# Performance work log

Hardware: AMD Instinct MI355X
Metric: run time of the kernel (lower is better)

## Reference

```python
import jax, jax.numpy as jnp
import numpy as np
import math

B, T, D, K, V = 8, 2048, 512, 512, 512


def setup_inputs() -> dict:
    key = jax.random.key(0)
    ks = jax.random.split(key, 4)
    minibatch = jax.random.normal(ks[0], (B, T, D), dtype=jnp.float32)
    # nn.Linear weights are [out, in]; biases [out]
    Wk = jax.random.normal(ks[1], (K, D), dtype=jnp.float32) * 0.02
    bk = jnp.zeros((K,), dtype=jnp.float32)
    Wq = jax.random.normal(ks[2], (K, D), dtype=jnp.float32) * 0.02
    bq = jnp.zeros((K,), dtype=jnp.float32)
    Wv = jax.random.normal(ks[3], (V, D), dtype=jnp.float32) * 0.02
    bv = jnp.zeros((V,), dtype=jnp.float32)
    return {"minibatch": minibatch, "Wk": Wk, "bk": bk, "Wq": Wq, "bq": bq, "Wv": Wv, "bv": bv}


def reference(minibatch, Wk, bk, Wq, bq, Wv, bv):
    k_size = Wk.shape[0]
    sqrt_k = math.sqrt(k_size)
    keys = jnp.einsum('btd,kd->btk', minibatch, Wk) + bk
    queries = jnp.einsum('btd,kd->btk', minibatch, Wq) + bq
    values = jnp.einsum('btd,vd->btv', minibatch, Wv) + bv
    # logits[b, t, s] = q_t . k_s
    logits = jnp.einsum('btk,bsk->bts', queries, keys)
    seq = minibatch.shape[1]
    # upper triangle (s > t) masked to -inf, matching np.triu(..., k=1)
    mask = jnp.triu(jnp.ones((seq, seq), dtype=bool), k=1)
    logits = jnp.where(mask[None, :, :], -jnp.inf, logits)
    # NOTE: original softmaxes over dim=1 (the query axis), then divides by sqrt(k)
    probs = jax.nn.softmax(logits, axis=1) / sqrt_k
    read = jnp.einsum('bts,bsv->btv', probs, values)
    return minibatch + read
```

## Files before the change

### kernel.cpp

```cpp
#include <hip/hip_runtime.h>


typedef __attribute__((ext_vector_type(4))) float f32x4;
typedef __attribute__((ext_vector_type(8))) short s16x8;
typedef __attribute__((ext_vector_type(4))) short s16x4;

#define SQRTK  22.627416997969522f

__device__ __forceinline__ short f2bf(float f) {
    union { float f; unsigned int i; } c; c.f = f;
    unsigned int x = c.i;
    return (short)((x + 0x7fffu + ((x >> 16) & 1u)) >> 16);
}
__device__ __forceinline__ void gll16(const void* g, void* l) {
    __builtin_amdgcn_global_load_lds(
        (const __attribute__((address_space(1))) void*)g,
        (__attribute__((address_space(3))) void*)l, 16, 0, 0);
}

__global__ __launch_bounds__(256) void k_cast(
    const float* __restrict__ in, unsigned short* __restrict__ out, int n4)
{
    int i = blockIdx.x * 256 + threadIdx.x;
    if (i >= n4) return;
    f32x4 v = *(const f32x4*)(in + (size_t)i * 4);
    s16x4 o;
#pragma unroll
    for (int j = 0; j < 4; ++j) o[j] = f2bf(v[j]);
    *(s16x4*)(out + (size_t)i * 4) = o;
}

__global__ __launch_bounds__(256) void k_castw(
    const float* __restrict__ q, const float* __restrict__ k, const float* __restrict__ v,
    unsigned short* __restrict__ oqk, unsigned short* __restrict__ ov)
{
    int i = blockIdx.x * 256 + threadIdx.x;
    const float* src; unsigned short* dst; int j;
    if (i < 65536)       { src = q; dst = oqk; j = i; }
    else if (i < 131072) { src = k; dst = oqk + 262144; j = i - 65536; }
    else                 { src = v; dst = ov; j = i - 131072; }
    f32x4 w = *(const f32x4*)(src + (size_t)j * 4);
    s16x4 o;
#pragma unroll
    for (int jj = 0; jj < 4; ++jj) o[jj] = f2bf(w[jj]);
    *(s16x4*)(dst + (size_t)j * 4) = o;
}

__global__ __launch_bounds__(256) void k_projqk(
    const unsigned short* __restrict__ Xb,
    const unsigned short* __restrict__ Wqk,
    const float* __restrict__ bq, const float* __restrict__ bk,
    unsigned short* __restrict__ C)
{
    __shared__ short la[2][128][32];
    __shared__ short lb[2][128][32];
    const int tid  = threadIdx.x;
    const int wave = tid >> 6, lane = tid & 63;
    const int wr = (wave >> 1) * 64, wc = (wave & 1) * 64;
    const int m0 = blockIdx.x * 128, n0 = blockIdx.y * 128;
    const int r0 = tid >> 2, c0 = (tid & 3) * 8;
    const int wvb = wave * 1024;
    const int frl = lane & 15, kb = (lane >> 4) * 8, rg4 = (lane >> 4) * 4;
    f32x4 acc[4][4] = {};

#define QK_STAGE(BUF, K0) { \
    char* pa_ = (char*)(&la[BUF][0][0]) + wvb; \
    char* pb_ = (char*)(&lb[BUF][0][0]) + wvb; \
    gll16(Xb  + (size_t)(m0 + r0) * 512 + (K0) + c0, pa_); \
    gll16(Xb  + (size_t)(m0 + r0 + 64) * 512 + (K0) + c0, pa_ + 4096); \
    gll16(Wqk + (size_t)(n0 + r0) * 512 + (K0) + c0, pb_); \
    gll16(Wqk + (size_t)(n0 + r0 + 64) * 512 + (K0) + c0, pb_ + 4096); }

    QK_STAGE(0, 0);
    __syncthreads();
    for (int ks = 0; ks < 16; ++ks) {
        const int cur = ks & 1;
        if (ks < 15) QK_STAGE(cur ^ 1, (ks + 1) * 32);
        s16x8 af[4], bfr[4];
#pragma unroll
        for (int i = 0; i < 4; ++i) af[i]  = *(const s16x8*)(&la[cur][wr + i * 16 + frl][kb]);
#pragma unroll
        for (int i = 0; i < 4; ++i) bfr[i] = *(const s16x8*)(&lb[cur][wc + i * 16 + frl][kb]);
#pragma unroll
        for (int mi = 0; mi < 4; ++mi)
#pragma unroll
            for (int ni = 0; ni < 4; ++ni)
                acc[mi][ni] = __builtin_amdgcn_mfma_f32_16x16x32_bf16(af[mi], bfr[ni], acc[mi][ni], 0, 0, 0);
        __syncthreads();
    }
#undef QK_STAGE
#pragma unroll
    for (int mi = 0; mi < 4; ++mi)
#pragma unroll
        for (int ni = 0; ni < 4; ++ni) {
            int col = n0 + wc + ni * 16 + frl;
            float bv = (col < 512) ? bq[col] : bk[col - 512];
#pragma unroll
            for (int r = 0; r < 4; ++r) {
                int row = m0 + wr + mi * 16 + rg4 + r;
                C[(size_t)row * 1024 + col] = f2bf(acc[mi][ni][r] + bv);
            }
        }
}

__global__ __launch_bounds__(256) void k_projv(
    const unsigned short* __restrict__ Wv,
    const unsigned short* __restrict__ Xb,
    const float* __restrict__ bv,
    const float* __restrict__ ft,
    unsigned short* __restrict__ C)
{
    __shared__ short la[2][128][32];
    __shared__ short lb[2][128][32];
    const int tid  = threadIdx.x;
    const int wave = tid >> 6, lane = tid & 63;
    const int wr = (wave >> 1) * 64, wc = (wave & 1) * 64;
    const int m0 = blockIdx.x * 128, n0 = blockIdx.y * 128;
    const int r0 = tid >> 2, c0 = (tid & 3) * 8;
    const int wvb = wave * 1024;
    const int frl = lane & 15, kb = (lane >> 4) * 8, rg4 = (lane >> 4) * 4;
    f32x4 acc[4][4] = {};

#define PV_STAGE(BUF, K0) { \
    char* pa_ = (char*)(&la[BUF][0][0]) + wvb; \
    char* pb_ = (char*)(&lb[BUF][0][0]) + wvb; \
    gll16(Wv + (size_t)(m0 + r0) * 512 + (K0) + c0, pa_); \
    gll16(Wv + (size_t)(m0 + r0 + 64) * 512 + (K0) + c0, pa_ + 4096); \
    gll16(Xb + (size_t)(n0 + r0) * 512 + (K0) + c0, pb_); \
    gll16(Xb + (size_t)(n0 + r0 + 64) * 512 + (K0) + c0, pb_ + 4096); }

    PV_STAGE(0, 0);
    __syncthreads();
    for (int ks = 0; ks < 16; ++ks) {
        const int cur = ks & 1;
        if (ks < 15) PV_STAGE(cur ^ 1, (ks + 1) * 32);
        s16x8 af[4], bfr[4];
#pragma unroll
        for (int i = 0; i < 4; ++i) af[i]  = *(const s16x8*)(&la[cur][wr + i * 16 + frl][kb]);
#pragma unroll
        for (int i = 0; i < 4; ++i) bfr[i] = *(const s16x8*)(&lb[cur][wc + i * 16 + frl][kb]);
#pragma unroll
        for (int mi = 0; mi < 4; ++mi)
#pragma unroll
            for (int ni = 0; ni < 4; ++ni)
                acc[mi][ni] = __builtin_amdgcn_mfma_f32_16x16x32_bf16(af[mi], bfr[ni], acc[mi][ni], 0, 0, 0);
        __syncthreads();
    }
#undef PV_STAGE
#pragma unroll
    for (int mi = 0; mi < 4; ++mi)
#pragma unroll
        for (int ni = 0; ni < 4; ++ni) {
            int col = n0 + wc + ni * 16 + frl;
            float fs = ft[col];
#pragma unroll
            for (int r = 0; r < 4; ++r) {
                int row = m0 + wr + mi * 16 + rg4 + r;
                C[(size_t)row * 16384 + col] = f2bf((acc[mi][ni][r] + bv[row]) * fs);
            }
        }
}

__global__ __launch_bounds__(256) void k_logits(
    const unsigned short* __restrict__ QK,
    unsigned short* __restrict__ Pc,
    float* __restrict__ pz)
{
    const int n = blockIdx.x;
    const int b = n & 7;
    const int p = n >> 3;
    int tt = (int)((sqrtf(8.f * p + 1.f) - 1.f) * 0.5f);
    while ((tt + 1) * (tt + 2) / 2 <= p) ++tt;
    while (tt * (tt + 1) / 2 > p) --tt;
    const int st = p - tt * (tt + 1) / 2;
    const int t0 = tt * 128, s0 = st * 128;

    const unsigned short* A  = QK + (size_t)b * 2048 * 1024;
    const unsigned short* Bt = QK + (size_t)b * 2048 * 1024 + 512;
    unsigned short* Pb = Pc + (size_t)b * 2048 * 2048;

    __shared__ short la[2][128][32];
    __shared__ short lb[2][128][32];
    __shared__ float sz[2][128];
    const int tid  = threadIdx.x;
    const int wave = tid >> 6, lane = tid & 63;
    const int wr = (wave >> 1) * 64, wc = (wave & 1) * 64;
    const int r0 = tid >> 2, c0 = (tid & 3) * 8;
    const int wvb = wave * 1024;
    const int frl = lane & 15, kb = (lane >> 4) * 8, rg4 = (lane >> 4) * 4;
    f32x4 acc[4][4] = {};

#define LG_STAGE(BUF, K0) { \
    char* pa_ = (char*)(&la[BUF][0][0]) + wvb; \
    char* pb_ = (char*)(&lb[BUF][0][0]) + wvb; \
    gll16(A  + (size_t)(t0 + r0) * 1024 + (K0) + c0, pa_); \
    gll16(A  + (size_t)(t0 + r0 + 64) * 1024 + (K0) + c0, pa_ + 4096); \
    gll16(Bt + (size_t)(s0 + r0) * 1024 + (K0) + c0, pb_); \
    gll16(Bt + (size_t)(s0 + r0 + 64) * 1024 + (K0) + c0, pb_ + 4096); }

    LG_STAGE(0, 0);
    __syncthreads();
    for (int ks = 0; ks < 16; ++ks) {
        const int cur = ks & 1;
        if (ks < 15) LG_STAGE(cur ^ 1, (ks + 1) * 32);
        s16x8 af[4], bfr[4];
#pragma unroll
        for (int i = 0; i < 4; ++i) af[i]  = *(const s16x8*)(&la[cur][wr + i * 16 + frl][kb]);
#pragma unroll
        for (int i = 0; i < 4; ++i) bfr[i] = *(const s16x8*)(&lb[cur][wc + i * 16 + frl][kb]);
#pragma unroll
        for (int mi = 0; mi < 4; ++mi)
#pragma unroll
            for (int ni = 0; ni < 4; ++ni)
                acc[mi][ni] = __builtin_amdgcn_mfma_f32_16x16x32_bf16(af[mi], bfr[ni], acc[mi][ni], 0, 0, 0);
        __syncthreads();
    }
#undef LG_STAGE

    float cz[4];
#pragma unroll
    for (int ni = 0; ni < 4; ++ni) {
        const int colg = s0 + wc + ni * 16 + frl;
        float zl = 0.f;
#pragma unroll
        for (int mi = 0; mi < 4; ++mi)
#pragma unroll
            for (int r = 0; r < 4; ++r) {
                int row = t0 + wr + mi * 16 + rg4 + r;
                float e = (colg <= row) ? __expf(acc[mi][ni][r]) : 0.f;
                acc[mi][ni][r] = e;
                zl += e;
            }
        zl += __shfl_xor(zl, 16);
        zl += __shfl_xor(zl, 32);
        cz[ni] = zl;
    }
    if (lane < 16) {
#pragma unroll
        for (int ni = 0; ni < 4; ++ni)
            sz[wr >> 6][wc + ni * 16 + lane] = cz[ni];
    }
    __syncthreads();
    if (tid < 128)
        pz[(b * 16 + tt) * 2048 + s0 + tid] = sz[0][tid] + sz[1][tid];
#pragma unroll
    for (int ni = 0; ni < 4; ++ni) {
        const int colg = s0 + wc + ni * 16 + frl;
#pragma unroll
        for (int mi = 0; mi < 4; ++mi)
#pragma unroll
            for (int r = 0; r < 4; ++r) {
                int row = t0 + wr + mi * 16 + rg4 + r;
                Pb[(size_t)row * 2048 + colg] = f2bf(acc[mi][ni][r]);
            }
    }
}

__global__ __launch_bounds__(256) void k_stats2(
    const float* __restrict__ pz, float* __restrict__ ft)
{
    const int i = blockIdx.x * 256 + threadIdx.x;
    const int b = i >> 11, s = i & 2047;
    float Z = 0.f;
    for (int tc = s >> 7; tc < 16; ++tc) Z += pz[(b * 16 + tc) * 2048 + s];
    ft[i] = 1.0f / (Z * SQRTK);
}

__global__ __launch_bounds__(256) void k_out(
    const unsigned short* __restrict__ Pc,
    const unsigned short* __restrict__ Vs,
    const float* __restrict__ X,
    float* __restrict__ Y)
{
    __shared__ short la[2][2][128][32];
    __shared__ short lb[2][2][128][32];
    const int n  = blockIdx.x;
    const int tt = 15 - (n >> 5);
    const int bv = n & 31;
    const int b = bv >> 2, v = bv & 3;
    const int t0 = tt * 128, v0 = v * 128;
    const unsigned short* Pb = Pc + (size_t)b * 2048 * 2048;
    const int tid  = threadIdx.x;
    const int wave = tid >> 6, lane = tid & 63;
    const int wr = (wave >> 1) * 64, wc = (wave & 1) * 64;
    const int frl = lane & 15, kb = (lane >> 4) * 8, rg4 = (lane >> 4) * 4;
    const int r0 = tid >> 2, c0 = (tid & 3) * 8;
    const int wvb = wave * 1024;

    f32x4 acc[4][4] = {};
    const int nit = (tt + 1) * 2;

#define OUT_STAGE(BUF, IT) { \
    int sb = (IT) * 64; \
    _Pragma("unroll") for (int h = 0; h < 2; ++h) { \
        char* pa_ = (char*)(&la[BUF][h][0][0]) + wvb; \
        char* pb_ = (char*)(&lb[BUF][h][0][0]) + wvb; \
        gll16(Pb + (size_t)(t0 + r0) * 2048 + sb + h * 32 + c0, pa_); \
        gll16(Pb + (size_t)(t0 + r0 + 64) * 2048 + sb + h * 32 + c0, pa_ + 4096); \
        gll16(Vs + (size_t)(v0 + r0) * 16384 + b * 2048 + sb + h * 32 + c0, pb_); \
        gll16(Vs + (size_t)(v0 + r0 + 64) * 16384 + b * 2048 + sb + h * 32 + c0, pb_ + 4096); } }

    OUT_STAGE(0, 0);
    __syncthreads();
    for (int it = 0; it < nit; ++it) {
        const int cur = it & 1;
        if (it + 1 < nit) OUT_STAGE(cur ^ 1, it + 1);
#pragma unroll
        for (int h = 0; h < 2; ++h) {
            s16x8 af[4], bfr[4];
#pragma unroll
            for (int i = 0; i < 4; ++i) af[i]  = *(const s16x8*)(&la[cur][h][wr + i * 16 + frl][kb]);
#pragma unroll
            for (int i = 0; i < 4; ++i) bfr[i] = *(const s16x8*)(&lb[cur][h][wc + i * 16 + frl][kb]);
#pragma unroll
            for (int mi = 0; mi < 4; ++mi)
#pragma unroll
                for (int ni = 0; ni < 4; ++ni)
                    acc[mi][ni] = __builtin_amdgcn_mfma_f32_16x16x32_bf16(af[mi], bfr[ni], acc[mi][ni], 0, 0, 0);
        }
        __syncthreads();
    }
#undef OUT_STAGE

#pragma unroll
    for (int mi = 0; mi < 4; ++mi)
#pragma unroll
        for (int ni = 0; ni < 4; ++ni) {
            int col = v0 + wc + ni * 16 + frl;
#pragma unroll
            for (int r = 0; r < 4; ++r) {
                int row = t0 + wr + mi * 16 + rg4 + r;
                size_t o = ((size_t)b * 2048 + row) * 512 + col;
                Y[o] = acc[mi][ni][r] + X[o];
            }
        }
}

extern "C" void kernel_launch(void* const* d_in, const int* in_sizes, int n_in,
                              void* d_out, int out_size, void* d_ws, size_t ws_size,
                              hipStream_t stream) {
    const float* Xf  = (const float*)d_in[0];
    const float* Wkf = (const float*)d_in[1];
    const float* bkf = (const float*)d_in[2];
    const float* Wqf = (const float*)d_in[3];
    const float* bqf = (const float*)d_in[4];
    const float* Wvf = (const float*)d_in[5];
    const float* bvf = (const float*)d_in[6];
    float* Y = (float*)d_out;
    char* ws = (char*)d_ws;

    float*          pz   = (float*)(ws);
    float*          ftab = (float*)(ws + 2097152);
    unsigned short* Wqkb = (unsigned short*)(ws + 4194304);
    unsigned short* Wvb  = (unsigned short*)(ws + 5242880);
    unsigned short* Xb   = (unsigned short*)(ws + 6291456);
    unsigned short* QKb  = (unsigned short*)(ws + 23068672);
    unsigned short* Vs   = (unsigned short*)(ws + 56623104);
    unsigned short* Pc   = (unsigned short*)(ws + 73400320);

    dim3 blk(256);
    k_cast<<<dim3(8192), blk, 0, stream>>>(Xf, Xb, 2097152);
    k_castw<<<dim3(768), blk, 0, stream>>>(Wqf, Wkf, Wvf, Wqkb, Wvb);
    k_projqk<<<dim3(128, 8), blk, 0, stream>>>(Xb, Wqkb, bqf, bkf, QKb);
    k_logits<<<dim3(1088), blk, 0, stream>>>(QKb, Pc, pz);
    k_stats2<<<dim3(64), blk, 0, stream>>>(pz, ftab);
    k_projv<<<dim3(4, 128), blk, 0, stream>>>(Wvb, Xb, bvf, ftab, Vs);
    k_out<<<dim3(512), blk, 0, stream>>>(Pc, Vs, Xf, Y);
}
```

Measured before the change: 144.5 us.

## Triple-buffer LDS pipeline with vmcnt waits in logits and output GEMMs

Replaces the double-buffered global_load_lds loops in k_logits and k_out with a three-stage ring buffer that prefetches two K-steps ahead. Each iteration waits only on the older loads through a partial s_waitcnt vmcnt plus a single s_barrier, instead of a full __syncthreads. k_out now uses 32-wide K steps instead of 64, which roughly halves its LDS footprint but doubles the iteration count and barrier frequency. MFMA blocks are wrapped in s_setprio to favour the math waves. The goal is to hide global-to-LDS latency behind compute, at the cost of relying on hand-counted vmcnt values that must match the four loads issued per stage.

```diff
diff --git a/kernel.cpp b/kernel.cpp
--- a/kernel.cpp
+++ b/kernel.cpp
@@ -179,8 +179,8 @@
     const unsigned short* Bt = QK + (size_t)b * 2048 * 1024 + 512;
     unsigned short* Pb = Pc + (size_t)b * 2048 * 2048;
 
-    __shared__ short la[2][128][32];
-    __shared__ short lb[2][128][32];
+    __shared__ short la[3][128][32];
+    __shared__ short lb[3][128][32];
     __shared__ float sz[2][128];
     const int tid  = threadIdx.x;
     const int wave = tid >> 6, lane = tid & 63;
@@ -199,21 +199,28 @@
     gll16(Bt + (size_t)(s0 + r0 + 64) * 1024 + (K0) + c0, pb_ + 4096); }
 
     LG_STAGE(0, 0);
-    __syncthreads();
+    LG_STAGE(1, 32);
+    int cur = 0;
     for (int ks = 0; ks < 16; ++ks) {
-        const int cur = ks & 1;
-        if (ks < 15) LG_STAGE(cur ^ 1, (ks + 1) * 32);
+        if (ks < 15) { asm volatile("s_waitcnt vmcnt(4)" ::: "memory"); }
+        else         { asm volatile("s_waitcnt vmcnt(0)" ::: "memory"); }
+        __builtin_amdgcn_sched_barrier(0);
+        __builtin_amdgcn_s_barrier();
+        __builtin_amdgcn_sched_barrier(0);
+        if (ks < 14) { int nb = cur + 2; if (nb >= 3) nb -= 3; LG_STAGE(nb, (ks + 2) * 32); }
         s16x8 af[4], bfr[4];
 #pragma unroll
         for (int i = 0; i < 4; ++i) af[i]  = *(const s16x8*)(&la[cur][wr + i * 16 + frl][kb]);
 #pragma unroll
         for (int i = 0; i < 4; ++i) bfr[i] = *(const s16x8*)(&lb[cur][wc + i * 16 + frl][kb]);
+        __builtin_amdgcn_s_setprio(1);
 #pragma unroll
         for (int mi = 0; mi < 4; ++mi)
 #pragma unroll
             for (int ni = 0; ni < 4; ++ni)
                 acc[mi][ni] = __builtin_amdgcn_mfma_f32_16x16x32_bf16(af[mi], bfr[ni], acc[mi][ni], 0, 0, 0);
-        __syncthreads();
+        __builtin_amdgcn_s_setprio(0);
+        cur = (cur == 2) ? 0 : cur + 1;
     }
 #undef LG_STAGE
 
@@ -272,8 +279,8 @@
     const float* __restrict__ X,
     float* __restrict__ Y)
 {
-    __shared__ short la[2][2][128][32];
-    __shared__ short lb[2][2][128][32];
+    __shared__ short la[3][128][32];
+    __shared__ short lb[3][128][32];
     const int n  = blockIdx.x;
     const int tt = 15 - (n >> 5);
     const int bv = n & 31;
@@ -288,37 +295,40 @@
     const int wvb = wave * 1024;
 
     f32x4 acc[4][4] = {};
-    const int nit = (tt + 1) * 2;
-
-#define OUT_STAGE(BUF, IT) { \
-    int sb = (IT) * 64; \
-    _Pragma("unroll") for (int h = 0; h < 2; ++h) { \
-        char* pa_ = (char*)(&la[BUF][h][0][0]) + wvb; \
-        char* pb_ = (char*)(&lb[BUF][h][0][0]) + wvb; \
-        gll16(Pb + (size_t)(t0 + r0) * 2048 + sb + h * 32 + c0, pa_); \
-        gll16(Pb + (size_t)(t0 + r0 + 64) * 2048 + sb + h * 32 + c0, pa_ + 4096); \
-        gll16(Vs + (size_t)(v0 + r0) * 16384 + b * 2048 + sb + h * 32 + c0, pb_); \
-        gll16(Vs + (size_t)(v0 + r0 + 64) * 16384 + b * 2048 + sb + h * 32 + c0, pb_ + 4096); } }
+    const int nit = (tt + 1) * 4;
+
+#define OUT_STAGE(BUF, IS) { \
+    int sb = (IS) * 32; \
+    char* pa_ = (char*)(&la[BUF][0][0]) + wvb; \
+    char* pb_ = (char*)(&lb[BUF][0][0]) + wvb; \
+    gll16(Pb + (size_t)(t0 + r0) * 2048 + sb + c0, pa_); \
+    gll16(Pb + (size_t)(t0 + r0 + 64) * 2048 + sb + c0, pa_ + 4096); \
+    gll16(Vs + (size_t)(v0 + r0) * 16384 + b * 2048 + sb + c0, pb_); \
+    gll16(Vs + (size_t)(v0 + r0 + 64) * 16384 + b * 2048 + sb + c0, pb_ + 4096); }
 
     OUT_STAGE(0, 0);
-    __syncthreads();
+    OUT_STAGE(1, 1);
+    int cur = 0;
     for (int it = 0; it < nit; ++it) {
-        const int cur = it & 1;
-        if (it + 1 < nit) OUT_STAGE(cur ^ 1, it + 1);
-#pragma unroll
-        for (int h = 0; h < 2; ++h) {
-            s16x8 af[4], bfr[4];
-#pragma unroll
-            for (int i = 0; i < 4; ++i) af[i]  = *(const s16x8*)(&la[cur][h][wr + i * 16 + frl][kb]);
-#pragma unroll
-            for (int i = 0; i < 4; ++i) bfr[i] = *(const s16x8*)(&lb[cur][h][wc + i * 16 + frl][kb]);
-#pragma unroll
-            for (int mi = 0; mi < 4; ++mi)
-#pragma unroll
-                for (int ni = 0; ni < 4; ++ni)
-                    acc[mi][ni] = __builtin_amdgcn_mfma_f32_16x16x32_bf16(af[mi], bfr[ni], acc[mi][ni], 0, 0, 0);
-        }
-        __syncthreads();
+        if (it + 1 < nit) { asm volatile("s_waitcnt vmcnt(4)" ::: "memory"); }
+        else              { asm volatile("s_waitcnt vmcnt(0)" ::: "memory"); }
+        __builtin_amdgcn_sched_barrier(0);
+        __builtin_amdgcn_s_barrier();
+        __builtin_amdgcn_sched_barrier(0);
+        if (it + 2 < nit) { int nb = cur + 2; if (nb >= 3) nb -= 3; OUT_STAGE(nb, it + 2); }
+        s16x8 af[4], bfr[4];
+#pragma unroll
+        for (int i = 0; i < 4; ++i) af[i]  = *(const s16x8*)(&la[cur][wr + i * 16 + frl][kb]);
+#pragma unroll
+        for (int i = 0; i < 4; ++i) bfr[i] = *(const s16x8*)(&lb[cur][wc + i * 16 + frl][kb]);
+        __builtin_amdgcn_s_setprio(1);
+#pragma unroll
+        for (int mi = 0; mi < 4; ++mi)
+#pragma unroll
+            for (int ni = 0; ni < 4; ++ni)
+                acc[mi][ni] = __builtin_amdgcn_mfma_f32_16x16x32_bf16(af[mi], bfr[ni], acc[mi][ni], 0, 0, 0);
+        __builtin_amdgcn_s_setprio(0);
+        cur = (cur == 2) ? 0 : cur + 1;
     }
 #undef OUT_STAGE
 
```

After: 151.3 us. 1.05x slower.

## Overlap next-tile global loads with MFMA via partial vmcnt waits

Applied to the files above, without the earlier changes.

In the logits and output GEMM loops, the full __syncthreads after the prefetch is replaced by an explicit s_waitcnt vmcnt(N). Each iteration waits only for the current buffer's async LDS loads, so the next stage's loads stay in flight during the MFMAs. Raw s_barrier with sched_barrier fences keep the compiler from reordering around the sync points, and s_setprio raises wave priority during MFMA bursts. This relies on the hand-counted vmcnt values matching the number of issued gll16 loads, which is fragile if load counts change.

```diff
diff --git a/kernel.cpp b/kernel.cpp
--- a/kernel.cpp
+++ b/kernel.cpp
@@ -199,21 +199,32 @@
     gll16(Bt + (size_t)(s0 + r0 + 64) * 1024 + (K0) + c0, pb_ + 4096); }
 
     LG_STAGE(0, 0);
-    __syncthreads();
     for (int ks = 0; ks < 16; ++ks) {
         const int cur = ks & 1;
-        if (ks < 15) LG_STAGE(cur ^ 1, (ks + 1) * 32);
+        if (ks < 15) {
+            LG_STAGE(cur ^ 1, (ks + 1) * 32);
+            asm volatile("s_waitcnt vmcnt(4)" ::: "memory");
+        } else {
+            asm volatile("s_waitcnt vmcnt(0)" ::: "memory");
+        }
+        __builtin_amdgcn_sched_barrier(0);
+        __builtin_amdgcn_s_barrier();
+        __builtin_amdgcn_sched_barrier(0);
         s16x8 af[4], bfr[4];
 #pragma unroll
         for (int i = 0; i < 4; ++i) af[i]  = *(const s16x8*)(&la[cur][wr + i * 16 + frl][kb]);
 #pragma unroll
         for (int i = 0; i < 4; ++i) bfr[i] = *(const s16x8*)(&lb[cur][wc + i * 16 + frl][kb]);
+        __builtin_amdgcn_s_setprio(1);
 #pragma unroll
         for (int mi = 0; mi < 4; ++mi)
 #pragma unroll
             for (int ni = 0; ni < 4; ++ni)
                 acc[mi][ni] = __builtin_amdgcn_mfma_f32_16x16x32_bf16(af[mi], bfr[ni], acc[mi][ni], 0, 0, 0);
-        __syncthreads();
+        __builtin_amdgcn_s_setprio(0);
+        __builtin_amdgcn_sched_barrier(0);
+        __builtin_amdgcn_s_barrier();
+        __builtin_amdgcn_sched_barrier(0);
     }
 #undef LG_STAGE
 
@@ -301,10 +312,17 @@
         gll16(Vs + (size_t)(v0 + r0 + 64) * 16384 + b * 2048 + sb + h * 32 + c0, pb_ + 4096); } }
 
     OUT_STAGE(0, 0);
-    __syncthreads();
     for (int it = 0; it < nit; ++it) {
         const int cur = it & 1;
-        if (it + 1 < nit) OUT_STAGE(cur ^ 1, it + 1);
+        if (it + 1 < nit) {
+            OUT_STAGE(cur ^ 1, it + 1);
+            asm volatile("s_waitcnt vmcnt(8)" ::: "memory");
+        } else {
+            asm volatile("s_waitcnt vmcnt(0)" ::: "memory");
+        }
+        __builtin_amdgcn_sched_barrier(0);
+        __builtin_amdgcn_s_barrier();
+        __builtin_amdgcn_sched_barrier(0);
 #pragma unroll
         for (int h = 0; h < 2; ++h) {
             s16x8 af[4], bfr[4];
@@ -312,13 +330,17 @@
             for (int i = 0; i < 4; ++i) af[i]  = *(const s16x8*)(&la[cur][h][wr + i * 16 + frl][kb]);
 #pragma unroll
             for (int i = 0; i < 4; ++i) bfr[i] = *(const s16x8*)(&lb[cur][h][wc + i * 16 + frl][kb]);
+            __builtin_amdgcn_s_setprio(1);
 #pragma unroll
             for (int mi = 0; mi < 4; ++mi)
 #pragma unroll
                 for (int ni = 0; ni < 4; ++ni)
                     acc[mi][ni] = __builtin_amdgcn_mfma_f32_16x16x32_bf16(af[mi], bfr[ni], acc[mi][ni], 0, 0, 0);
-        }
-        __syncthreads();
+            __builtin_amdgcn_s_setprio(0);
+        }
+        __builtin_amdgcn_sched_barrier(0);
+        __builtin_amdgcn_s_barrier();
+        __builtin_amdgcn_sched_barrier(0);
     }
 #undef OUT_STAGE
 
```

Measured after the change: 148.2 us. 2.6% more time.
